# Kernel optimization log

Hardware: AMD Instinct MI355X
Metric: run time of the kernel (lower is better)

## Reference

```python
import jax, jax.numpy as jnp
import numpy as np

NUM_USERS = 100000
NUM_ITEMS = 50000
NUM_EDGES = 2000000
DIM = 64
NUM_REL = 5


def setup_inputs() -> dict:
    key = jax.random.key(0)
    k1, k2, k3, k4, k5, k6 = jax.random.split(key, 6)
    u_features = jax.random.normal(k1, (NUM_USERS, DIM), dtype=jnp.float32)
    i_features = jax.random.normal(k2, (NUM_ITEMS, DIM), dtype=jnp.float32)
    edge_user = jax.random.randint(k3, (NUM_EDGES,), 0, NUM_USERS, dtype=jnp.int64)
    edge_item = jax.random.randint(k4, (NUM_EDGES,), 0, NUM_ITEMS, dtype=jnp.int64)
    # per-relation Linear params, torch convention: y = x @ W[r].T + b[r]
    W = jax.random.normal(k5, (NUM_REL, DIM, DIM), dtype=jnp.float32) * (1.0 / np.sqrt(DIM))
    b = jax.random.normal(k6, (NUM_REL, DIM), dtype=jnp.float32) * 0.01
    return {"u_features": u_features, "i_features": i_features,
            "edge_user": edge_user, "edge_item": edge_item, "W": W, "b": b}


def reference(u_features, i_features, edge_user, edge_item, W, b):
    # gather edge endpoint features: [E, D]
    edge_u = u_features[edge_user]
    edge_i = i_features[edge_item]
    num_rel = W.shape[0]
    # per relation: sum((edge_u @ W[r].T + b[r]) * edge_i, axis=1) -> [E]
    # loop over small fixed relation count to avoid [E, R, D] intermediate
    cols = [jnp.sum((edge_u @ W[r].T + b[r]) * edge_i, axis=1)
            for r in range(num_rel)]
    return jnp.stack(cols, axis=1)  # [E, R]
```

## Files before the change

kernel.cpp:

```cpp
#include <hip/hip_runtime.h>
#include <stdint.h>

#define NREL 5
#define D 64
#define Q_BYTES 320
#define NT 21
#define NB 8
#define CHUNK 2048

typedef __attribute__((ext_vector_type(8))) short short8;
typedef __attribute__((ext_vector_type(4))) float f32x4;

static __device__ __forceinline__ short f2bf(float f) {
    uint32_t u = __float_as_uint(f);
    u += 0x7FFFu + ((u >> 16) & 1u);
    return (short)(u >> 16);
}

#if defined(__has_builtin)
#if __has_builtin(__builtin_amdgcn_sdot4)
#define HAVE_SDOT4 1
#endif
#endif
#ifdef HAVE_SDOT4
static __device__ __forceinline__ int SDOT4(uint32_t a, uint32_t b, int c) {
    return __builtin_amdgcn_sdot4((int)a, (int)b, c, false);
}
#else
static __device__ __forceinline__ int SDOT4(uint32_t a, uint32_t b, int c) {
    c += ((int)(a << 24) >> 24) * ((int)(b << 24) >> 24);
    c += ((int)(a << 16) >> 24) * ((int)(b << 16) >> 24);
    c += ((int)(a << 8) >> 24) * ((int)(b << 8) >> 24);
    c += ((int)a >> 24) * ((int)b >> 24);
    return c;
}
#endif

__global__ __launch_bounds__(256) void w_prep_kernel(
    const float* __restrict__ W, const float* __restrict__ b, short* __restrict__ Wf)
{
    const int tid = blockIdx.x * 256 + threadIdx.x;
    if (tid >= NT * 2 * 64) return;
    const int lane = tid & 63;
    const int h = (tid >> 6) & 1;
    const int nt = tid >> 7;
    const int ln = lane & 15, quad = lane >> 4;
    const int n = nt * 16 + ln;
    uint32_t w[4];
#pragma unroll
    for (int p = 0; p < 4; ++p) {
        uint32_t lo = 0, hi = 0;
#pragma unroll
        for (int s = 0; s < 2; ++s) {
            const int j = p * 2 + s;
            const int d = h * 32 + quad * 8 + j;
            float v;
            if (nt < 20) v = W[(n >> 6) * (D * D) + d * D + (n & 63)];
            else         v = (ln < NREL) ? b[ln * D + d] : 0.f;
            if (s == 0) lo = (uint16_t)f2bf(v); else hi = (uint16_t)f2bf(v);
        }
        w[p] = lo | (hi << 16);
    }
    *(uint4*)(Wf + (size_t)tid * 8) = make_uint4(w[0], w[1], w[2], w[3]);
}

__global__ __launch_bounds__(256) void u_quant_kernel(
    const float* __restrict__ uf,
    uint32_t* __restrict__ uq,
    float* __restrict__ uscale,
    int nRows)
{
    const int gid = blockIdx.x * 256 + threadIdx.x;
    const int row = gid >> 4;
    const int t = gid & 15;
    if (row >= nRows) return;
    const float* rp = uf + (size_t)row * D;
    const float v0 = rp[t], v1 = rp[16 + t], v2 = rp[32 + t], v3 = rp[48 + t];
    float m = fmaxf(fmaxf(fabsf(v0), fabsf(v1)), fmaxf(fabsf(v2), fabsf(v3)));
    m = fmaxf(m, __shfl_xor(m, 1));
    m = fmaxf(m, __shfl_xor(m, 2));
    m = fmaxf(m, __shfl_xor(m, 4));
    m = fmaxf(m, __shfl_xor(m, 8));
    m = fmaxf(m, 1e-20f);
    const float qs = 127.0f / m;
    const int q0 = (int)rintf(v0 * qs);
    const int q1 = (int)rintf(v1 * qs);
    const int q2 = (int)rintf(v2 * qs);
    const int q3 = (int)rintf(v3 * qs);
    uq[(size_t)row * 16 + t] = ((uint32_t)(uint8_t)(int8_t)q0)
                             | ((uint32_t)(uint8_t)(int8_t)q1 << 8)
                             | ((uint32_t)(uint8_t)(int8_t)q2 << 16)
                             | ((uint32_t)(uint8_t)(int8_t)q3 << 24);
    if (t == 0) uscale[row] = m * (1.0f / 127.0f);
}

__global__ __launch_bounds__(256) void item_transform_kernel(
    const float* __restrict__ i_feat,
    const short* __restrict__ Wf,
    char* __restrict__ qrecs,
    float* __restrict__ sc,
    int nItems)
{
    const int lane = threadIdx.x & 63;
    const int wv = threadIdx.x >> 6;
    const int m0 = blockIdx.x * 64 + wv * 16;
    const int ln = lane & 15, quad = lane >> 4;

    int rowA = m0 + ln;
    if (rowA >= nItems) rowA = nItems - 1;
    const float* ap = i_feat + (size_t)rowA * D + quad * 8;
    short8 af[2];
#pragma unroll
    for (int h = 0; h < 2; ++h) {
        const float4 x = *(const float4*)(ap + h * 32);
        const float4 y = *(const float4*)(ap + h * 32 + 4);
        short8 a;
        a[0] = f2bf(x.x); a[1] = f2bf(x.y); a[2] = f2bf(x.z); a[3] = f2bf(x.w);
        a[4] = f2bf(y.x); a[5] = f2bf(y.y); a[6] = f2bf(y.z); a[7] = f2bf(y.w);
        af[h] = a;
    }

    f32x4 acc[NT];
#pragma unroll
    for (int nt = 0; nt < NT; ++nt) acc[nt] = (f32x4){0.f, 0.f, 0.f, 0.f};

#pragma unroll
    for (int nt = 0; nt < NT; ++nt) {
        const short8 b0 = *(const short8*)(Wf + ((size_t)(nt * 2 + 0) * 64 + lane) * 8);
        acc[nt] = __builtin_amdgcn_mfma_f32_16x16x32_bf16(af[0], b0, acc[nt], 0, 0, 0);
        const short8 b1 = *(const short8*)(Wf + ((size_t)(nt * 2 + 1) * 64 + lane) * 8);
        acc[nt] = __builtin_amdgcn_mfma_f32_16x16x32_bf16(af[1], b1, acc[nt], 0, 0, 0);
    }

#pragma unroll
    for (int g = 0; g < 4; ++g) {
        const int item = m0 + quad * 4 + g;
        const bool ok = (item < nItems);
        char* rec = qrecs + (size_t)item * Q_BYTES;
#pragma unroll
        for (int r = 0; r < NREL; ++r) {
            const float v0 = acc[4 * r + 0][g];
            const float v1 = acc[4 * r + 1][g];
            const float v2 = acc[4 * r + 2][g];
            const float v3 = acc[4 * r + 3][g];
            float m = fmaxf(fmaxf(fabsf(v0), fabsf(v1)), fmaxf(fabsf(v2), fabsf(v3)));
            m = fmaxf(m, __shfl_xor(m, 1));
            m = fmaxf(m, __shfl_xor(m, 2));
            m = fmaxf(m, __shfl_xor(m, 4));
            m = fmaxf(m, __shfl_xor(m, 8));
            m = fmaxf(m, 1e-20f);
            const float qs = 127.0f / m;
            const uint32_t pw = ((uint32_t)(uint8_t)(int8_t)(int)rintf(v0 * qs))
                              | ((uint32_t)(uint8_t)(int8_t)(int)rintf(v1 * qs) << 8)
                              | ((uint32_t)(uint8_t)(int8_t)(int)rintf(v2 * qs) << 16)
                              | ((uint32_t)(uint8_t)(int8_t)(int)rintf(v3 * qs) << 24);
            if (ok) {
                *(uint32_t*)(rec + r * D + ln * 4) = pw;
                if (ln == 0) sc[(size_t)item * 16 + r] = m * (1.0f / 127.0f);
            }
        }
        if (ok && ln < NREL) sc[(size_t)item * 16 + NREL + ln] = acc[20][g];
    }
}

__global__ __launch_bounds__(256) void hist_kernel(
    const int* __restrict__ edge_item, int nE, int bucketDiv,
    int* __restrict__ blkHist)
{
    __shared__ int cnt[NB];
    if (threadIdx.x < NB) cnt[threadIdx.x] = 0;
    __syncthreads();
    const long start = (long)blockIdx.x * CHUNK;
#pragma unroll
    for (int k = 0; k < CHUNK / 256; ++k) {
        const long e = start + k * 256 + threadIdx.x;
        if (e < nE) atomicAdd(&cnt[edge_item[e] / bucketDiv], 1);
    }
    __syncthreads();
    if (threadIdx.x < NB) blkHist[blockIdx.x * NB + threadIdx.x] = cnt[threadIdx.x];
}

__global__ __launch_bounds__(512) void scan_kernel(
    int* __restrict__ blkHist, int nBlocks, int* __restrict__ bucketBase)
{
    __shared__ int tot[NB];
    __shared__ int base[NB + 1];
    const int lane = threadIdx.x & 63;
    const int b = threadIdx.x >> 6;
    int carry = 0;
    for (int c0 = 0; c0 < nBlocks; c0 += 64) {
        const int idx = c0 + lane;
        int v = (idx < nBlocks) ? blkHist[idx * NB + b] : 0;
        int s = v;
#pragma unroll
        for (int d = 1; d < 64; d <<= 1) {
            int t = __shfl_up(s, d);
            if (lane >= d) s += t;
        }
        if (idx < nBlocks) blkHist[idx * NB + b] = carry + s - v;
        carry += __shfl(s, 63);
    }
    if (lane == 0) tot[b] = carry;
    __syncthreads();
    if (threadIdx.x == 0) {
        int s = 0;
#pragma unroll
        for (int i = 0; i < NB; ++i) { base[i] = s; s += tot[i]; }
        base[NB] = s;
#pragma unroll
        for (int i = 0; i <= NB; ++i) bucketBase[i] = base[i];
    }
    __syncthreads();
    const int add = base[b];
    for (int c0 = 0; c0 < nBlocks; c0 += 64) {
        const int idx = c0 + lane;
        if (idx < nBlocks) blkHist[idx * NB + b] += add;
    }
}

__global__ __launch_bounds__(256) void scatter_kernel(
    const int* __restrict__ edge_user, const int* __restrict__ edge_item,
    int nE, int bucketDiv, const int* __restrict__ blkHist,
    unsigned long long* __restrict__ sorted)
{
    __shared__ int cnt[NB];
    __shared__ int base[NB];
    if (threadIdx.x < NB) {
        cnt[threadIdx.x] = 0;
        base[threadIdx.x] = blkHist[blockIdx.x * NB + threadIdx.x];
    }
    __syncthreads();
    const long start = (long)blockIdx.x * CHUNK;
#pragma unroll
    for (int k = 0; k < CHUNK / 256; ++k) {
        const long e = start + k * 256 + threadIdx.x;
        if (e < nE) {
            const int iu = edge_user[e];
            const int ii = edge_item[e];
            const int b = ii / bucketDiv;
            const int rank = atomicAdd(&cnt[b], 1);
            const unsigned long long pk = (unsigned long long)(uint32_t)iu
                                        | ((unsigned long long)(uint32_t)ii << 17)
                                        | ((unsigned long long)e << 33);
            sorted[base[b] + rank] = pk;
        }
    }
}

__global__ __launch_bounds__(256) void edge_kernel(
    const uint32_t* __restrict__ u_q,
    const float* __restrict__ u_scale,
    const unsigned long long* __restrict__ sorted,
    const int* __restrict__ bucketBase,
    const char* __restrict__ qrecs,
    const float* __restrict__ sc,
    float* __restrict__ out)
{
    const int b = blockIdx.x & 7;
    const int seg = blockIdx.x >> 3;
    const int nSeg = gridDim.x >> 3;
    const int s0 = bucketBase[b], s1 = bucketBase[b + 1];
    const int cnt = s1 - s0;
    const int per = (cnt + nSeg - 1) / nSeg;
    const int p0 = s0 + seg * per;
    const int p1 = min(p0 + per, s1);

    const int lane = threadIdx.x & 63;
    const int wv = threadIdx.x >> 6;
    const int es = lane >> 2;
    const int c = lane & 3;

    for (int q0 = p0 + wv * 16; q0 < p1; q0 += 64) {
        const int pos = q0 + es;
        if (pos < p1) {
            const unsigned long long pk = sorted[pos];
            const int iu = (int)(pk & 0x1FFFF);
            const int ii = (int)((pk >> 17) & 0xFFFF);
            const long e = (long)(pk >> 33);

            const uint4 uv = *(const uint4*)(u_q + (size_t)iu * 16 + c * 4);
            const char* rec = qrecs + (size_t)ii * Q_BYTES;

            int s[NREL];
#pragma unroll
            for (int r = 0; r < NREL; ++r) {
                const uint4 yv = *(const uint4*)(rec + r * D + c * 16);
                int t = SDOT4(uv.x, yv.x, 0);
                t = SDOT4(uv.y, yv.y, t);
                t = SDOT4(uv.z, yv.z, t);
                s[r] = SDOT4(uv.w, yv.w, t);
            }
#pragma unroll
            for (int r = 0; r < NREL; ++r) {
                s[r] += __shfl_xor(s[r], 1);
                s[r] += __shfl_xor(s[r], 2);
            }
            const float us = u_scale[iu];
            const float* scp = sc + (size_t)ii * 16;
            out[e * NREL + c] = fmaf((float)s[c], us * scp[c], scp[NREL + c]);
            if (c == 0)
                out[e * NREL + 4] = fmaf((float)s[4], us * scp[4], scp[NREL + 4]);
        }
    }
}

extern "C" void kernel_launch(void* const* d_in, const int* in_sizes, int n_in,
                              void* d_out, int out_size, void* d_ws, size_t ws_size,
                              hipStream_t stream) {
    const float* u_feat    = (const float*)d_in[0];
    const float* i_feat    = (const float*)d_in[1];
    const int*   edge_user = (const int*)d_in[2];
    const int*   edge_item = (const int*)d_in[3];
    const float* W         = (const float*)d_in[4];
    const float* b         = (const float*)d_in[5];
    float* out = (float*)d_out;

    const int nUsers = in_sizes[0] / D;
    const int nItems = in_sizes[1] / D;
    const int nE = in_sizes[2];
    const int bucketDiv = (nItems + NB - 1) / NB;
    const int nBlocksSort = (nE + CHUNK - 1) / CHUNK;

    size_t off = 0;
    char* qrecs = (char*)d_ws;
    off += ((size_t)nItems * Q_BYTES + 255) & ~(size_t)255;
    float* sc = (float*)((char*)d_ws + off);
    off += ((size_t)nItems * 16 * sizeof(float) + 255) & ~(size_t)255;
    uint32_t* u_q = (uint32_t*)((char*)d_ws + off);
    off += ((size_t)nUsers * D + 255) & ~(size_t)255;
    float* u_scale = (float*)((char*)d_ws + off);
    off += ((size_t)nUsers * sizeof(float) + 255) & ~(size_t)255;
    short* Wf = (short*)((char*)d_ws + off);
    off += ((size_t)NT * 2 * 64 * 8 * sizeof(short) + 255) & ~(size_t)255;
    int* blkHist = (int*)((char*)d_ws + off);
    off += ((size_t)nBlocksSort * NB * sizeof(int) + 255) & ~(size_t)255;
    int* bucketBase = (int*)((char*)d_ws + off);
    off += 256;
    unsigned long long* sorted = (unsigned long long*)((char*)d_ws + off);

    {
        const int threads = NT * 2 * 64;
        w_prep_kernel<<<(threads + 255) / 256, 256, 0, stream>>>(W, b, Wf);
    }
    {
        const int threads = nUsers * 16;
        u_quant_kernel<<<(threads + 255) / 256, 256, 0, stream>>>(u_feat, u_q, u_scale, nUsers);
    }
    {
        const int blocks = (nItems + 63) / 64;
        item_transform_kernel<<<blocks, 256, 0, stream>>>(i_feat, Wf, qrecs, sc, nItems);
    }
    hist_kernel<<<nBlocksSort, 256, 0, stream>>>(edge_item, nE, bucketDiv, blkHist);
    scan_kernel<<<1, 512, 0, stream>>>(blkHist, nBlocksSort, bucketBase);
    scatter_kernel<<<nBlocksSort, 256, 0, stream>>>(edge_user, edge_item, nE, bucketDiv,
                                                    blkHist, sorted);
    edge_kernel<<<1280, 256, 0, stream>>>(u_q, u_scale, sorted, bucketBase,
                                          qrecs, sc, out);
}
```

Measured before the change: 277.6 us.

## Fuse prep kernels, sub-bucket edges by user range, prefetch sorted edges

```diff
diff --git a/kernel.cpp b/kernel.cpp
--- a/kernel.cpp
+++ b/kernel.cpp
@@ -6,7 +6,10 @@
 #define Q_BYTES 320
 #define NT 21
 #define NB 8
+#define NSUB 16
+#define NBT (NB * NSUB)
 #define CHUNK 2048
+#define EDGE_GRID 2048
 
 typedef __attribute__((ext_vector_type(8))) short short8;
 typedef __attribute__((ext_vector_type(4))) float f32x4;
@@ -36,62 +39,87 @@
 }
 #endif
 
-__global__ __launch_bounds__(256) void w_prep_kernel(
-    const float* __restrict__ W, const float* __restrict__ b, short* __restrict__ Wf)
-{
-    const int tid = blockIdx.x * 256 + threadIdx.x;
-    if (tid >= NT * 2 * 64) return;
-    const int lane = tid & 63;
-    const int h = (tid >> 6) & 1;
-    const int nt = tid >> 7;
-    const int ln = lane & 15, quad = lane >> 4;
-    const int n = nt * 16 + ln;
-    uint32_t w[4];
-#pragma unroll
-    for (int p = 0; p < 4; ++p) {
-        uint32_t lo = 0, hi = 0;
-#pragma unroll
-        for (int s = 0; s < 2; ++s) {
-            const int j = p * 2 + s;
-            const int d = h * 32 + quad * 8 + j;
-            float v;
-            if (nt < 20) v = W[(n >> 6) * (D * D) + d * D + (n & 63)];
-            else         v = (ln < NREL) ? b[ln * D + d] : 0.f;
-            if (s == 0) lo = (uint16_t)f2bf(v); else hi = (uint16_t)f2bf(v);
-        }
-        w[p] = lo | (hi << 16);
-    }
-    *(uint4*)(Wf + (size_t)tid * 8) = make_uint4(w[0], w[1], w[2], w[3]);
-}
-
-__global__ __launch_bounds__(256) void u_quant_kernel(
-    const float* __restrict__ uf,
-    uint32_t* __restrict__ uq,
-    float* __restrict__ uscale,
-    int nRows)
-{
-    const int gid = blockIdx.x * 256 + threadIdx.x;
-    const int row = gid >> 4;
-    const int t = gid & 15;
-    if (row >= nRows) return;
-    const float* rp = uf + (size_t)row * D;
-    const float v0 = rp[t], v1 = rp[16 + t], v2 = rp[32 + t], v3 = rp[48 + t];
-    float m = fmaxf(fmaxf(fabsf(v0), fabsf(v1)), fmaxf(fabsf(v2), fabsf(v3)));
-    m = fmaxf(m, __shfl_xor(m, 1));
-    m = fmaxf(m, __shfl_xor(m, 2));
-    m = fmaxf(m, __shfl_xor(m, 4));
-    m = fmaxf(m, __shfl_xor(m, 8));
-    m = fmaxf(m, 1e-20f);
-    const float qs = 127.0f / m;
-    const int q0 = (int)rintf(v0 * qs);
-    const int q1 = (int)rintf(v1 * qs);
-    const int q2 = (int)rintf(v2 * qs);
-    const int q3 = (int)rintf(v3 * qs);
-    uq[(size_t)row * 16 + t] = ((uint32_t)(uint8_t)(int8_t)q0)
-                             | ((uint32_t)(uint8_t)(int8_t)q1 << 8)
-                             | ((uint32_t)(uint8_t)(int8_t)q2 << 16)
-                             | ((uint32_t)(uint8_t)(int8_t)q3 << 24);
-    if (t == 0) uscale[row] = m * (1.0f / 127.0f);
+__global__ __launch_bounds__(256) void prep_kernel(
+    const float* __restrict__ W, const float* __restrict__ bias_p, short* __restrict__ Wf,
+    const float* __restrict__ uf, uint32_t* __restrict__ uq, float* __restrict__ uscale,
+    int nUsers,
+    const int* __restrict__ edge_item, const int* __restrict__ edge_user,
+    int nE, int bucketDiv, int subDiv, int* __restrict__ blkHist, int nBlocksSort)
+{
+    __shared__ int cnt[NBT];
+    const int nbW = (NT * 2 * 64 + 255) / 256;
+    const int nbU = (nUsers * 16 + 255) / 256;
+    int bid = blockIdx.x;
+
+    if (bid < nbW) {
+        const int tid = bid * 256 + threadIdx.x;
+        if (tid >= NT * 2 * 64) return;
+        const int lane = tid & 63;
+        const int h = (tid >> 6) & 1;
+        const int nt = tid >> 7;
+        const int ln = lane & 15, quad = lane >> 4;
+        const int n = nt * 16 + ln;
+        uint32_t w[4];
+#pragma unroll
+        for (int p = 0; p < 4; ++p) {
+            uint32_t lo = 0, hi = 0;
+#pragma unroll
+            for (int s = 0; s < 2; ++s) {
+                const int j = p * 2 + s;
+                const int d = h * 32 + quad * 8 + j;
+                float v;
+                if (nt < 20) v = W[(n >> 6) * (D * D) + d * D + (n & 63)];
+                else         v = (ln < NREL) ? bias_p[ln * D + d] : 0.f;
+                if (s == 0) lo = (uint16_t)f2bf(v); else hi = (uint16_t)f2bf(v);
+            }
+            w[p] = lo | (hi << 16);
+        }
+        *(uint4*)(Wf + (size_t)tid * 8) = make_uint4(w[0], w[1], w[2], w[3]);
+        return;
+    }
+    bid -= nbW;
+
+    if (bid < nbU) {
+        const int gid = bid * 256 + threadIdx.x;
+        const int row = gid >> 4;
+        const int t = gid & 15;
+        if (row >= nUsers) return;
+        const float* rp = uf + (size_t)row * D;
+        const float v0 = rp[t], v1 = rp[16 + t], v2 = rp[32 + t], v3 = rp[48 + t];
+        float m = fmaxf(fmaxf(fabsf(v0), fabsf(v1)), fmaxf(fabsf(v2), fabsf(v3)));
+        m = fmaxf(m, __shfl_xor(m, 1));
+        m = fmaxf(m, __shfl_xor(m, 2));
+        m = fmaxf(m, __shfl_xor(m, 4));
+        m = fmaxf(m, __shfl_xor(m, 8));
+        m = fmaxf(m, 1e-20f);
+        const float qs = 127.0f / m;
+        const int q0 = (int)rintf(v0 * qs);
+        const int q1 = (int)rintf(v1 * qs);
+        const int q2 = (int)rintf(v2 * qs);
+        const int q3 = (int)rintf(v3 * qs);
+        uq[(size_t)row * 16 + t] = ((uint32_t)(uint8_t)(int8_t)q0)
+                                 | ((uint32_t)(uint8_t)(int8_t)q1 << 8)
+                                 | ((uint32_t)(uint8_t)(int8_t)q2 << 16)
+                                 | ((uint32_t)(uint8_t)(int8_t)q3 << 24);
+        if (t == 0) uscale[row] = m * (1.0f / 127.0f);
+        return;
+    }
+    bid -= nbU;
+
+    if (threadIdx.x < NBT) cnt[threadIdx.x] = 0;
+    __syncthreads();
+    const long start = (long)bid * CHUNK;
+#pragma unroll
+    for (int k = 0; k < CHUNK / 256; ++k) {
+        const long e = start + k * 256 + threadIdx.x;
+        if (e < nE) {
+            const int ii = edge_item[e];
+            const int iu = edge_user[e];
+            atomicAdd(&cnt[(ii / bucketDiv) * NSUB + (iu / subDiv)], 1);
+        }
+    }
+    __syncthreads();
+    if (threadIdx.x < NBT) blkHist[(size_t)threadIdx.x * nBlocksSort + bid] = cnt[threadIdx.x];
 }
 
 __global__ __launch_bounds__(256) void item_transform_kernel(
@@ -156,78 +184,70 @@
                               | ((uint32_t)(uint8_t)(int8_t)(int)rintf(v3 * qs) << 24);
             if (ok) {
                 *(uint32_t*)(rec + r * D + ln * 4) = pw;
-                if (ln == 0) sc[(size_t)item * 16 + r] = m * (1.0f / 127.0f);
-            }
-        }
-        if (ok && ln < NREL) sc[(size_t)item * 16 + NREL + ln] = acc[20][g];
-    }
-}
-
-__global__ __launch_bounds__(256) void hist_kernel(
-    const int* __restrict__ edge_item, int nE, int bucketDiv,
-    int* __restrict__ blkHist)
-{
-    __shared__ int cnt[NB];
-    if (threadIdx.x < NB) cnt[threadIdx.x] = 0;
-    __syncthreads();
-    const long start = (long)blockIdx.x * CHUNK;
-#pragma unroll
-    for (int k = 0; k < CHUNK / 256; ++k) {
-        const long e = start + k * 256 + threadIdx.x;
-        if (e < nE) atomicAdd(&cnt[edge_item[e] / bucketDiv], 1);
-    }
-    __syncthreads();
-    if (threadIdx.x < NB) blkHist[blockIdx.x * NB + threadIdx.x] = cnt[threadIdx.x];
-}
-
-__global__ __launch_bounds__(512) void scan_kernel(
+                if (ln == 0) sc[(size_t)item * 16 + 2 * r] = m * (1.0f / 127.0f);
+            }
+        }
+        if (ok && ln < NREL) sc[(size_t)item * 16 + 2 * ln + 1] = acc[20][g];
+    }
+}
+
+__global__ __launch_bounds__(1024) void scan_kernel(
     int* __restrict__ blkHist, int nBlocks, int* __restrict__ bucketBase)
 {
-    __shared__ int tot[NB];
-    __shared__ int base[NB + 1];
+    __shared__ int tot[NBT];
+    __shared__ int base[NBT + 1];
     const int lane = threadIdx.x & 63;
-    const int b = threadIdx.x >> 6;
-    int carry = 0;
-    for (int c0 = 0; c0 < nBlocks; c0 += 64) {
-        const int idx = c0 + lane;
-        int v = (idx < nBlocks) ? blkHist[idx * NB + b] : 0;
-        int s = v;
-#pragma unroll
-        for (int d = 1; d < 64; d <<= 1) {
-            int t = __shfl_up(s, d);
-            if (lane >= d) s += t;
-        }
-        if (idx < nBlocks) blkHist[idx * NB + b] = carry + s - v;
-        carry += __shfl(s, 63);
-    }
-    if (lane == 0) tot[b] = carry;
+    const int w = threadIdx.x >> 6;
+#pragma unroll
+    for (int cc = 0; cc < NBT / 16; ++cc) {
+        const int b = w * (NBT / 16) + cc;
+        int* col = blkHist + (size_t)b * nBlocks;
+        int carry = 0;
+        for (int c0 = 0; c0 < nBlocks; c0 += 64) {
+            const int idx = c0 + lane;
+            int v = (idx < nBlocks) ? col[idx] : 0;
+            int s = v;
+#pragma unroll
+            for (int d = 1; d < 64; d <<= 1) {
+                int t = __shfl_up(s, d);
+                if (lane >= d) s += t;
+            }
+            if (idx < nBlocks) col[idx] = carry + s - v;
+            carry += __shfl(s, 63);
+        }
+        if (lane == 0) tot[b] = carry;
+    }
     __syncthreads();
     if (threadIdx.x == 0) {
         int s = 0;
 #pragma unroll
-        for (int i = 0; i < NB; ++i) { base[i] = s; s += tot[i]; }
-        base[NB] = s;
-#pragma unroll
-        for (int i = 0; i <= NB; ++i) bucketBase[i] = base[i];
-    }
-    __syncthreads();
-    const int add = base[b];
-    for (int c0 = 0; c0 < nBlocks; c0 += 64) {
-        const int idx = c0 + lane;
-        if (idx < nBlocks) blkHist[idx * NB + b] += add;
+        for (int i = 0; i < NBT; ++i) { base[i] = s; s += tot[i]; }
+        base[NBT] = s;
+        for (int i = 0; i <= NBT; ++i) bucketBase[i] = base[i];
+    }
+    __syncthreads();
+#pragma unroll
+    for (int cc = 0; cc < NBT / 16; ++cc) {
+        const int b = w * (NBT / 16) + cc;
+        const int add = base[b];
+        int* col = blkHist + (size_t)b * nBlocks;
+        for (int c0 = 0; c0 < nBlocks; c0 += 64) {
+            const int idx = c0 + lane;
+            if (idx < nBlocks) col[idx] += add;
+        }
     }
 }
 
 __global__ __launch_bounds__(256) void scatter_kernel(
     const int* __restrict__ edge_user, const int* __restrict__ edge_item,
-    int nE, int bucketDiv, const int* __restrict__ blkHist,
+    int nE, int bucketDiv, int subDiv, const int* __restrict__ blkHist, int nBlocksSort,
     unsigned long long* __restrict__ sorted)
 {
-    __shared__ int cnt[NB];
-    __shared__ int base[NB];
-    if (threadIdx.x < NB) {
+    __shared__ int cnt[NBT];
+    __shared__ int base[NBT];
+    if (threadIdx.x < NBT) {
         cnt[threadIdx.x] = 0;
-        base[threadIdx.x] = blkHist[blockIdx.x * NB + threadIdx.x];
+        base[threadIdx.x] = blkHist[(size_t)threadIdx.x * nBlocksSort + blockIdx.x];
     }
     __syncthreads();
     const long start = (long)blockIdx.x * CHUNK;
@@ -237,12 +257,12 @@
         if (e < nE) {
             const int iu = edge_user[e];
             const int ii = edge_item[e];
-            const int b = ii / bucketDiv;
-            const int rank = atomicAdd(&cnt[b], 1);
+            const int kb = (ii / bucketDiv) * NSUB + (iu / subDiv);
+            const int rank = atomicAdd(&cnt[kb], 1);
             const unsigned long long pk = (unsigned long long)(uint32_t)iu
                                         | ((unsigned long long)(uint32_t)ii << 17)
                                         | ((unsigned long long)e << 33);
-            sorted[base[b] + rank] = pk;
+            sorted[base[kb] + rank] = pk;
         }
     }
 }
@@ -259,21 +279,26 @@
     const int b = blockIdx.x & 7;
     const int seg = blockIdx.x >> 3;
     const int nSeg = gridDim.x >> 3;
-    const int s0 = bucketBase[b], s1 = bucketBase[b + 1];
-    const int cnt = s1 - s0;
-    const int per = (cnt + nSeg - 1) / nSeg;
-    const int p0 = s0 + seg * per;
-    const int p1 = min(p0 + per, s1);
+    const int s0 = bucketBase[b * NSUB];
+    const int s1 = bucketBase[(b + 1) * NSUB];
 
     const int lane = threadIdx.x & 63;
     const int wv = threadIdx.x >> 6;
     const int es = lane >> 2;
     const int c = lane & 3;
-
-    for (int q0 = p0 + wv * 16; q0 < p1; q0 += 64) {
-        const int pos = q0 + es;
-        if (pos < p1) {
-            const unsigned long long pk = sorted[pos];
+    const int stride = nSeg * 64;
+
+    int q0 = s0 + seg * 64 + wv * 16;
+    if (q0 >= s1) return;
+    int pos = q0 + es;
+    unsigned long long pk = (pos < s1) ? __builtin_nontemporal_load(sorted + pos) : 0ull;
+
+    for (; q0 < s1; q0 += stride) {
+        const int posn = q0 + stride + es;
+        const unsigned long long pkn =
+            (posn < s1 && q0 + stride < s1) ? __builtin_nontemporal_load(sorted + posn) : 0ull;
+
+        if (q0 + es < s1) {
             const int iu = (int)(pk & 0x1FFFF);
             const int ii = (int)((pk >> 17) & 0xFFFF);
             const long e = (long)(pk >> 33);
@@ -297,10 +322,16 @@
             }
             const float us = u_scale[iu];
             const float* scp = sc + (size_t)ii * 16;
-            out[e * NREL + c] = fmaf((float)s[c], us * scp[c], scp[NREL + c]);
-            if (c == 0)
-                out[e * NREL + 4] = fmaf((float)s[4], us * scp[4], scp[NREL + 4]);
-        }
+            const float2 sb = *(const float2*)(scp + 2 * c);
+            __builtin_nontemporal_store(fmaf((float)s[c], us * sb.x, sb.y),
+                                        out + e * NREL + c);
+            if (c == 0) {
+                const float2 sb4 = *(const float2*)(scp + 8);
+                __builtin_nontemporal_store(fmaf((float)s[4], us * sb4.x, sb4.y),
+                                            out + e * NREL + 4);
+            }
+        }
+        pk = pkn;
     }
 }
 
@@ -319,6 +350,7 @@
     const int nItems = in_sizes[1] / D;
     const int nE = in_sizes[2];
     const int bucketDiv = (nItems + NB - 1) / NB;
+    const int subDiv = (nUsers + NSUB - 1) / NSUB;
     const int nBlocksSort = (nE + CHUNK - 1) / CHUNK;
 
     size_t off = 0;
@@ -333,27 +365,20 @@
     short* Wf = (short*)((char*)d_ws + off);
     off += ((size_t)NT * 2 * 64 * 8 * sizeof(short) + 255) & ~(size_t)255;
     int* blkHist = (int*)((char*)d_ws + off);
-    off += ((size_t)nBlocksSort * NB * sizeof(int) + 255) & ~(size_t)255;
+    off += ((size_t)NBT * nBlocksSort * sizeof(int) + 255) & ~(size_t)255;
     int* bucketBase = (int*)((char*)d_ws + off);
-    off += 256;
+    off += 1024;
     unsigned long long* sorted = (unsigned long long*)((char*)d_ws + off);
 
-    {
-        const int threads = NT * 2 * 64;
-        w_prep_kernel<<<(threads + 255) / 256, 256, 0, stream>>>(W, b, Wf);
-    }
-    {
-        const int threads = nUsers * 16;
-        u_quant_kernel<<<(threads + 255) / 256, 256, 0, stream>>>(u_feat, u_q, u_scale, nUsers);
-    }
-    {
-        const int blocks = (nItems + 63) / 64;
-        item_transform_kernel<<<blocks, 256, 0, stream>>>(i_feat, Wf, qrecs, sc, nItems);
-    }
-    hist_kernel<<<nBlocksSort, 256, 0, stream>>>(edge_item, nE, bucketDiv, blkHist);
-    scan_kernel<<<1, 512, 0, stream>>>(blkHist, nBlocksSort, bucketBase);
-    scatter_kernel<<<nBlocksSort, 256, 0, stream>>>(edge_user, edge_item, nE, bucketDiv,
-                                                    blkHist, sorted);
-    edge_kernel<<<1280, 256, 0, stream>>>(u_q, u_scale, sorted, bucketBase,
-                                          qrecs, sc, out);
-}
+    const int nbW = (NT * 2 * 64 + 255) / 256;
+    const int nbU = (nUsers * 16 + 255) / 256;
+    prep_kernel<<<nbW + nbU + nBlocksSort, 256, 0, stream>>>(
+        W, b, Wf, u_feat, u_q, u_scale, nUsers,
+        edge_item, edge_user, nE, bucketDiv, subDiv, blkHist, nBlocksSort);
+    item_transform_kernel<<<(nItems + 63) / 64, 256, 0, stream>>>(i_feat, Wf, qrecs, sc, nItems);
+    scan_kernel<<<1, 1024, 0, stream>>>(blkHist, nBlocksSort, bucketBase);
+    scatter_kernel<<<nBlocksSort, 256, 0, stream>>>(edge_user, edge_item, nE, bucketDiv, subDiv,
+                                                    blkHist, nBlocksSort, sorted);
+    edge_kernel<<<EDGE_GRID, 256, 0, stream>>>(u_q, u_scale, sorted, bucketBase,
+                                               qrecs, sc, out);
+}
```

Result: slower. 392.3 us (+41.3%).
